# Kernel tuning notes

Hardware: AMD Instinct MI355X
Metric: run time of the kernel (lower is better)

Reference implementation:

```python
import jax, jax.numpy as jnp
import numpy as np

B, K, D, H, L = 128, 128, 768, 8, 4
HD = D // H
FF = 4 * D
SIM = D // 4
BOOST = 0.3
SCALE = HD ** -0.5
EPS = 1e-5


def _ln(x, g, b):
    m = x.mean(-1, keepdims=True)
    v = ((x - m) ** 2).mean(-1, keepdims=True)
    return (x - m) * jax.lax.rsqrt(v + EPS) * g + b


def setup_inputs() -> dict:
    key = jax.random.key(0)
    ks = jax.random.split(key, 10)
    def n(k, shape, s=0.02):
        return jax.random.normal(k, shape, dtype=jnp.float32) * s
    return {
        'slots': jax.random.normal(ks[0], (B, K, D), dtype=jnp.float32),
        'pos_emb': n(ks[1], (1, K, D)),
        'Wq': n(ks[2], (L, D, D)),
        'Wk': n(ks[3], (L, D, D)),
        'Wv': n(ks[4], (L, D, D)),
        'Wo': n(ks[5], (L, D, D)),
        'bo': jnp.zeros((L, D), jnp.float32),
        'Wsim': n(ks[6], (L, D, SIM)),
        'g1': jnp.ones((L, D), jnp.float32),
        'b1': jnp.zeros((L, D), jnp.float32),
        'g2': jnp.ones((L, D), jnp.float32),
        'b2': jnp.zeros((L, D), jnp.float32),
        'Wff1': n(ks[7], (L, D, FF)),
        'bff1': jnp.zeros((L, FF), jnp.float32),
        'Wff2': n(ks[8], (L, FF, D)),
        'bff2': jnp.zeros((L, D), jnp.float32),
        'gf': jnp.ones((D,), jnp.float32),
        'bf': jnp.zeros((D,), jnp.float32),
    }


def reference(slots, pos_emb, Wq, Wk, Wv, Wo, bo, Wsim, g1, b1, g2, b2,
              Wff1, bff1, Wff2, bff2, gf, bf):
    x = slots + pos_emb  # K == max_slots -> full pos table
    for l in range(L):
        # --- similarity-biased multi-head self-attention (pre-norm) ---
        nx = _ln(x, g1[l], b1[l])
        q = (nx @ Wq[l]).reshape(B, K, H, HD)
        k = (nx @ Wk[l]).reshape(B, K, H, HD)
        v = (nx @ Wv[l]).reshape(B, K, H, HD)
        scores = jnp.einsum('bqhd,bkhd->bhqk', q, k) * SCALE  # [B,H,K,K]
        s = nx @ Wsim[l]  # [B,K,D/4]
        s = s / jnp.maximum(jnp.linalg.norm(s, axis=-1, keepdims=True), 1e-12)
        sim = jnp.einsum('bqc,bkc->bqk', s, s)  # cosine similarity matrix
        scores = scores + BOOST * sim[:, None, :, :]
        a = jax.nn.softmax(scores, axis=-1)
        o = jnp.einsum('bhqk,bkhd->bqhd', a, v).reshape(B, K, D)
        x = x + (o @ Wo[l] + bo[l])
        # --- feed-forward (pre-norm) ---
        nx = _ln(x, g2[l], b2[l])
        h = jax.nn.gelu(nx @ Wff1[l] + bff1[l], approximate=False)
        x = x + (h @ Wff2[l] + bff2[l])
    return _ln(x, gf, bf)
```

## Files before the change

kernel.cpp:

```cpp
#include <hip/hip_runtime.h>

typedef unsigned short u16;
typedef unsigned int u32;
typedef float f32x4 __attribute__((ext_vector_type(4)));
typedef __bf16 bf16x8 __attribute__((ext_vector_type(8)));

static constexpr int D = 768, FFD = 3072, SIMC = 192, NH = 8, HD = 96;
static constexpr int B = 128, K = 128, M = B * K, NL = 4;
static constexpr int QKVW = 2560;
static constexpr int SIMOFF = 2304;
static constexpr float QSCALE = 0.14724502f;
static constexpr float SBOOST2 = 0.6578821f;
static constexpr float EPS_F = 1e-5f;

__device__ __forceinline__ float bf2f(u16 u) {
  union { u32 i; float f; } v; v.i = ((u32)u) << 16; return v.f;
}
__device__ __forceinline__ u16 f2bf(float f) {
  union { float f; u32 i; } v; v.f = f;
  u32 u = v.i;
  u32 r = (u + 0x7FFFu + ((u >> 16) & 1u)) >> 16;
  return (u16)r;
}

__device__ __forceinline__ float fast_gelu(float x) {
  float u2 = x * (2.3020585f + 0.102944f * x * x);
  float e = __builtin_amdgcn_exp2f(u2);
  float r = __builtin_amdgcn_rcpf(1.0f + e);
  return x - x * r;
}

__device__ __forceinline__ void gload16(const void* g, void* l) {
  __builtin_amdgcn_global_load_lds(
      (const __attribute__((address_space(1))) void*)g,
      (__attribute__((address_space(3))) void*)l, 16, 0, 0);
}

__global__ __launch_bounds__(256) void addpos_kernel(
    const float* __restrict__ slots, const float* __restrict__ pos,
    u16* __restrict__ x) {
  int i = blockIdx.x * 256 + threadIdx.x;
  int m = i / D;
  int d = i - m * D;
  x[i] = f2bf(slots[i] + pos[(m & (K - 1)) * D + d]);
}

__device__ __forceinline__ float block_sum(float v, float* sbuf) {
#pragma unroll
  for (int off = 32; off > 0; off >>= 1) v += __shfl_xor(v, off, 64);
  int lane = threadIdx.x & 63, w = threadIdx.x >> 6;
  if (lane == 0) sbuf[w] = v;
  __syncthreads();
  v = sbuf[0] + sbuf[1] + sbuf[2] + sbuf[3];
  __syncthreads();
  return v;
}

template <bool OUT_BF16>
__global__ __launch_bounds__(256) void ln_kernel(
    const u16* __restrict__ x, const float* __restrict__ g,
    const float* __restrict__ b, void* __restrict__ out) {
  __shared__ float sbuf[4];
  int row = blockIdx.x, tid = threadIdx.x;
  const u16* xr = x + (size_t)row * D;
  float v0 = bf2f(xr[tid]), v1 = bf2f(xr[tid + 256]), v2 = bf2f(xr[tid + 512]);
  float s = block_sum(v0 + v1 + v2, sbuf);
  float mean = s * (1.0f / D);
  float d0 = v0 - mean, d1 = v1 - mean, d2 = v2 - mean;
  float sq = block_sum(d0 * d0 + d1 * d1 + d2 * d2, sbuf);
  float rs = rsqrtf(sq * (1.0f / D) + EPS_F);
  float y0 = d0 * rs * g[tid] + b[tid];
  float y1 = d1 * rs * g[tid + 256] + b[tid + 256];
  float y2 = d2 * rs * g[tid + 512] + b[tid + 512];
  if (OUT_BF16) {
    u16* o = (u16*)out + (size_t)row * D;
    o[tid] = f2bf(y0); o[tid + 256] = f2bf(y1); o[tid + 512] = f2bf(y2);
  } else {
    float* o = (float*)out + (size_t)row * D;
    o[tid] = y0; o[tid + 256] = y1; o[tid + 512] = y2;
  }
}

struct WAll {
  const float *wq, *wk, *wv, *wo, *wsim, *wff1, *wff2;
  u16 *tA, *tB, *tC, *tD;
};
__global__ __launch_bounds__(256) void wconv_all_kernel(WAll p, float qscale) {
  __shared__ u16 t[32][33];
  int bid = blockIdx.x;
  int l = bid / 7056, b = bid - l * 7056;
  const float* W; u16* Wt; int N, Kd, n0, k0;
  float sc = 1.0f;
  if (b < 2304) {
    int z = b / 576, rem = b - z * 576;
    N = 768; Kd = 768;
    n0 = (rem % 24) * 32; k0 = (rem / 24) * 32;
    if (z == 0) { W = p.wq + (size_t)l * 589824; Wt = p.tA + (size_t)l * 1966080; sc = qscale; }
    else if (z == 1) { W = p.wk + (size_t)l * 589824; Wt = p.tA + (size_t)l * 1966080 + 589824; }
    else if (z == 2) { W = p.wv + (size_t)l * 589824; Wt = p.tA + (size_t)l * 1966080 + 1179648; }
    else { W = p.wo + (size_t)l * 589824; Wt = p.tB + (size_t)l * 589824; }
  } else if (b < 2448) {
    int rem = b - 2304;
    W = p.wsim + (size_t)l * 147456;
    Wt = p.tA + (size_t)l * 1966080 + (size_t)SIMOFF * 768;
    N = SIMC; Kd = 768;
    n0 = (rem % 6) * 32; k0 = (rem / 6) * 32;
  } else if (b < 4752) {
    int rem = b - 2448;
    W = p.wff1 + (size_t)l * 2359296; Wt = p.tC + (size_t)l * 2359296;
    N = FFD; Kd = 768;
    n0 = (rem % 96) * 32; k0 = (rem / 96) * 32;
  } else {
    int rem = b - 4752;
    W = p.wff2 + (size_t)l * 2359296; Wt = p.tD + (size_t)l * 2359296;
    N = 768; Kd = FFD;
    n0 = (rem % 24) * 32; k0 = (rem / 24) * 32;
  }
  int tid = threadIdx.x;
  int c = tid & 31, r4 = tid >> 5;
#pragma unroll
  for (int i = 0; i < 4; ++i) {
    int r = r4 + i * 8;
    t[r][c] = f2bf(W[(size_t)(k0 + r) * N + n0 + c] * sc);
  }
  __syncthreads();
#pragma unroll
  for (int i = 0; i < 4; ++i) {
    int r = r4 + i * 8;
    Wt[(size_t)(n0 + r) * Kd + k0 + c] = t[c][r];
  }
}

template <bool BIAS, bool GELU_, bool RESID>
__global__ __launch_bounds__(512, 2) void gemm256_kernel(
    const u16* __restrict__ A, const u16* __restrict__ Bt,
    const float* __restrict__ bias, const u16* __restrict__ resid,
    u16* __restrict__ Cout, int N, int Kdim, int NBX) {
  __shared__ u16 lds[65536];
  int tid = threadIdx.x;
  int w = tid >> 6, lane = tid & 63;
  int wm = w >> 2, wn = w & 3;
  int lr = lane & 15, lg = lane >> 4;

  int nwg = gridDim.x;
  int cpx = nwg >> 3;
  int swz = (blockIdx.x & 7) * cpx + (blockIdx.x >> 3);
  int bx = swz % NBX, by = swz / NBX;
  int n0 = bx << 8, m0 = by << 8;

  int scol = ((lane & 7) ^ (lane >> 3)) << 3;
  size_t aOff = (size_t)((w << 4) + (lane >> 3)) * Kdim + scol;
  u16* ldsU = lds;

  auto stageA = [&](int buf, int h, int t) {
    const u16* g = A + (size_t)(m0 + (h << 7)) * Kdim + ((size_t)t << 6) + aOff;
    u16* l = ldsU + buf * 32768 + h * 8192 + (w << 10);
    gload16(g, l);
    gload16(g + ((size_t)Kdim << 3), l + 512);
  };
  auto stageB = [&](int buf, int h, int t) {
    const u16* g = Bt + (size_t)(n0 + (h << 7)) * Kdim + ((size_t)t << 6) + aOff;
    u16* l = ldsU + buf * 32768 + 16384 + h * 8192 + (w << 10);
    gload16(g, l);
    gload16(g + ((size_t)Kdim << 3), l + 512);
  };

  const u16* lA0p = ldsU;
  const u16* lB0p = ldsU + 16384;
  const u16* lA1p = ldsU + 32768;
  const u16* lB1p = ldsU + 49152;
  int arow = (wm * 128 + lr) * 64;
  int brow = (wn * 64 + lr) * 64;
  int swz0 = (((lg * 16)) ^ ((lr & 7) << 4)) >> 1;
  int swz1 = ((64 + lg * 16) ^ ((lr & 7) << 4)) >> 1;

  f32x4 acc[8][4] = {};
  bf16x8 ar[2][4], br[2][4];

#define READ_A_KS(BASE, MSEG, KS)                                            \
  do {                                                                       \
    _Pragma("unroll") for (int mm = 0; mm < 4; ++mm) {                       \
      const u16* p_ = (BASE) + arow + ((MSEG) * 64 + mm * 16) * 64;          \
      ar[KS][mm] = *(const bf16x8*)(p_ + ((KS) ? swz1 : swz0));              \
    }                                                                        \
  } while (0)
#define READ_B_KS(BASE, NSEG, KS)                                            \
  do {                                                                       \
    _Pragma("unroll") for (int nn = 0; nn < 2; ++nn) {                       \
      const u16* p_ = (BASE) + brow + ((NSEG) * 32 + nn * 16) * 64;          \
      br[KS][(NSEG) * 2 + nn] = *(const bf16x8*)(p_ + ((KS) ? swz1 : swz0)); \
    }                                                                        \
  } while (0)
#define MFMA_Q(MSEG, NSEG)                                                   \
  do {                                                                       \
    __builtin_amdgcn_s_setprio(1);                                           \
    _Pragma("unroll") for (int ks = 0; ks < 2; ++ks)                         \
      _Pragma("unroll") for (int mm = 0; mm < 4; ++mm)                       \
        _Pragma("unroll") for (int nn = 0; nn < 2; ++nn)                     \
          acc[(MSEG) * 4 + mm][(NSEG) * 2 + nn] =                            \
              __builtin_amdgcn_mfma_f32_16x16x32_bf16(                       \
                  ar[ks][mm], br[ks][(NSEG) * 2 + nn],                       \
                  acc[(MSEG) * 4 + mm][(NSEG) * 2 + nn], 0, 0, 0);           \
    __builtin_amdgcn_s_setprio(0);                                           \
  } while (0)
#define PSYNC()                                                              \
  do {                                                                       \
    __builtin_amdgcn_sched_barrier(0);                                       \
    asm volatile("s_waitcnt lgkmcnt(0)" ::: "memory");                       \
    __builtin_amdgcn_s_barrier();                                            \
    __builtin_amdgcn_sched_barrier(0);                                       \
  } while (0)
#define PSYNC_V(N)                                                           \
  do {                                                                       \
    __builtin_amdgcn_sched_barrier(0);                                       \
    asm volatile("s_waitcnt vmcnt(" #N ") lgkmcnt(0)" ::: "memory");         \
    __builtin_amdgcn_s_barrier();                                            \
    __builtin_amdgcn_sched_barrier(0);                                       \
  } while (0)

  int NK = Kdim >> 6, NI = NK >> 1;
  stageA(0, 0, 0); stageA(0, 1, 0); stageB(0, 0, 0); stageB(0, 1, 0);
  stageB(1, 0, 1); stageB(1, 1, 1);
  asm volatile("s_waitcnt vmcnt(4)" ::: "memory");
  __builtin_amdgcn_s_barrier();
  __builtin_amdgcn_sched_barrier(0);

  for (int i = 0; i < NI; ++i) {
    int t1 = 2 * i + 1, t2 = 2 * i + 2, t3 = 2 * i + 3;
    bool last = (i == NI - 1);
    stageA(1, 0, t1); stageA(1, 1, t1);
    READ_A_KS(lA0p, 0, 0); READ_B_KS(lB0p, 0, 0); READ_B_KS(lB0p, 1, 0);
    READ_A_KS(lA0p, 0, 1); READ_B_KS(lB0p, 0, 1); READ_B_KS(lB0p, 1, 1);
    MFMA_Q(0, 0); MFMA_Q(0, 1);
    PSYNC();
    if (!last) { stageB(0, 0, t2); stageB(0, 1, t2); }
    READ_A_KS(lA0p, 1, 0); READ_A_KS(lA0p, 1, 1);
    MFMA_Q(1, 0); MFMA_Q(1, 1);
    if (last) PSYNC_V(0);
    else      PSYNC_V(4);
    if (!last) { stageA(0, 0, t2); stageA(0, 1, t2); }
    READ_A_KS(lA1p, 0, 0); READ_B_KS(lB1p, 0, 0); READ_B_KS(lB1p, 1, 0);
    READ_A_KS(lA1p, 0, 1); READ_B_KS(lB1p, 0, 1); READ_B_KS(lB1p, 1, 1);
    MFMA_Q(0, 0); MFMA_Q(0, 1);
    PSYNC();
    if (!last) { stageB(1, 0, t3); stageB(1, 1, t3); }
    READ_A_KS(lA1p, 1, 0); READ_A_KS(lA1p, 1, 1);
    MFMA_Q(1, 0); MFMA_Q(1, 1);
    if (last) PSYNC();
    else      PSYNC_V(4);
  }

#pragma unroll
  for (int m = 0; m < 8; ++m) {
#pragma unroll
    for (int n = 0; n < 4; ++n) {
      int col = n0 + wn * 64 + n * 16 + lr;
      float bv = BIAS ? bias[col] : 0.0f;
#pragma unroll
      for (int r = 0; r < 4; ++r) {
        int row = m0 + wm * 128 + m * 16 + lg * 4 + r;
        float v = acc[m][n][r];
        if (BIAS) v += bv;
        if (GELU_) v = fast_gelu(v);
        if (RESID) v += bf2f(resid[(size_t)row * N + col]);
        Cout[(size_t)row * N + col] = f2bf(v);
      }
    }
  }
#undef READ_A_KS
#undef READ_B_KS
#undef MFMA_Q
#undef PSYNC
#undef PSYNC_V
}

__global__ __launch_bounds__(256) void simpre_kernel(
    const u16* __restrict__ qkvb, u16* __restrict__ psim) {
  __shared__ u16 sln[128][200];
  int b = blockIdx.x, tid = threadIdx.x;
  {
    int row = tid >> 1, half = tid & 1;
    const u16* sr = qkvb + ((size_t)(b * K + row)) * QKVW + SIMOFF + half * 96;
    u16 v[96];
    float sq = 0.f;
#pragma unroll
    for (int j = 0; j < 12; ++j) {
      uint4 u4 = *(const uint4*)(sr + j * 8);
      u32 uu[4] = {u4.x, u4.y, u4.z, u4.w};
#pragma unroll
      for (int t = 0; t < 4; ++t) {
        v[j * 8 + 2 * t] = (u16)(uu[t] & 0xffffu);
        v[j * 8 + 2 * t + 1] = (u16)(uu[t] >> 16);
      }
    }
#pragma unroll
    for (int j = 0; j < 96; ++j) { float f = bf2f(v[j]); sq += f * f; }
    sq += __shfl_xor(sq, 1, 64);
    float inv = SBOOST2 / fmaxf(sqrtf(sq), 1e-12f);
#pragma unroll
    for (int j = 0; j < 96; ++j) sln[row][half * 96 + j] = f2bf(bf2f(v[j]) * inv);
  }
  __syncthreads();
  int w = tid >> 6, lane = tid & 63;
  int lr = lane & 15, lg = lane >> 4;
  int q0 = 32 * w;
  f32x4 accs[2][8] = {};
#pragma unroll
  for (int ks = 0; ks < 6; ++ks) {
    bf16x8 af[2];
#pragma unroll
    for (int m = 0; m < 2; ++m)
      af[m] = *(const bf16x8*)(&sln[q0 + 16 * m + lr][ks * 32 + lg * 8]);
#pragma unroll
    for (int n = 0; n < 8; ++n) {
      bf16x8 bf = *(const bf16x8*)(&sln[16 * n + lr][ks * 32 + lg * 8]);
#pragma unroll
      for (int m = 0; m < 2; ++m)
        accs[m][n] = __builtin_amdgcn_mfma_f32_16x16x32_bf16(af[m], bf, accs[m][n], 0, 0, 0);
    }
  }
  u16* pb = psim + (size_t)b * K * K;
#pragma unroll
  for (int m = 0; m < 2; ++m)
#pragma unroll
    for (int n = 0; n < 8; ++n)
#pragma unroll
      for (int r = 0; r < 4; ++r)
        pb[(size_t)(q0 + 16 * m + 4 * lg + r) * K + 16 * n + lr] = f2bf(accs[m][n][r]);
}

__global__ __launch_bounds__(256) void attn_kernel(
    const u16* __restrict__ qkv, const u16* __restrict__ psim,
    u16* __restrict__ ob) {
  __shared__ u16 Vt[96][136];
  __shared__ u16 Pl[4][32][136];
  int bh = blockIdx.x, b = bh >> 3, h = bh & 7;
  int tid = threadIdx.x, w = tid >> 6, lane = tid & 63;
  int lr = lane & 15, lg = lane >> 4;
  const u16* qb = qkv + (size_t)b * K * QKVW + h * HD;
  const u16* kb = qb + D;
  const u16* vb = qb + 2 * D;
  for (int idx = tid; idx < 128 * 12; idx += 256) {
    int r = idx / 12, db = idx - r * 12;
    uint4 v4 = *(const uint4*)(vb + (size_t)r * QKVW + db * 8);
    u32 vv[4] = {v4.x, v4.y, v4.z, v4.w};
#pragma unroll
    for (int j = 0; j < 4; ++j) {
      Vt[db * 8 + 2 * j][r] = (u16)(vv[j] & 0xffffu);
      Vt[db * 8 + 2 * j + 1][r] = (u16)(vv[j] >> 16);
    }
  }
  u16* siml = &Pl[0][0][0];
  {
    const u16* pb = psim + (size_t)b * K * K;
    for (int c = tid; c < 2048; c += 256) {
      int r = c >> 4, cc = c & 15;
      *(uint4*)(siml + r * 136 + cc * 8) = *(const uint4*)(pb + r * 128 + cc * 8);
    }
  }
  __syncthreads();
  int q0 = 32 * w;
  f32x4 accs[2][8];
#pragma unroll
  for (int m = 0; m < 2; ++m)
#pragma unroll
    for (int n = 0; n < 8; ++n)
#pragma unroll
      for (int r = 0; r < 4; ++r)
        accs[m][n][r] = bf2f(siml[(q0 + 16 * m + 4 * lg + r) * 136 + 16 * n + lr]);
#pragma unroll
  for (int ks = 0; ks < 3; ++ks) {
    bf16x8 af[2];
#pragma unroll
    for (int m = 0; m < 2; ++m)
      af[m] = *(const bf16x8*)(qb + (size_t)(q0 + 16 * m + lr) * QKVW + ks * 32 + lg * 8);
#pragma unroll
    for (int n = 0; n < 8; ++n) {
      bf16x8 bf = *(const bf16x8*)(kb + (size_t)(16 * n + lr) * QKVW + ks * 32 + lg * 8);
#pragma unroll
      for (int m = 0; m < 2; ++m)
        accs[m][n] = __builtin_amdgcn_mfma_f32_16x16x32_bf16(af[m], bf, accs[m][n], 0, 0, 0);
    }
  }
#pragma unroll
  for (int m = 0; m < 2; ++m) {
    float mx[4] = {-3e38f, -3e38f, -3e38f, -3e38f};
#pragma unroll
    for (int n = 0; n < 8; ++n)
#pragma unroll
      for (int r = 0; r < 4; ++r) mx[r] = fmaxf(mx[r], accs[m][n][r]);
#pragma unroll
    for (int r = 0; r < 4; ++r) {
      mx[r] = fmaxf(mx[r], __shfl_xor(mx[r], 1, 64));
      mx[r] = fmaxf(mx[r], __shfl_xor(mx[r], 2, 64));
      mx[r] = fmaxf(mx[r], __shfl_xor(mx[r], 4, 64));
      mx[r] = fmaxf(mx[r], __shfl_xor(mx[r], 8, 64));
    }
    float sm[4] = {0.f, 0.f, 0.f, 0.f};
#pragma unroll
    for (int n = 0; n < 8; ++n)
#pragma unroll
      for (int r = 0; r < 4; ++r) {
        float e = __builtin_amdgcn_exp2f(accs[m][n][r] - mx[r]);
        accs[m][n][r] = e;
        sm[r] += e;
      }
#pragma unroll
    for (int r = 0; r < 4; ++r) {
      sm[r] += __shfl_xor(sm[r], 1, 64);
      sm[r] += __shfl_xor(sm[r], 2, 64);
      sm[r] += __shfl_xor(sm[r], 4, 64);
      sm[r] += __shfl_xor(sm[r], 8, 64);
    }
    float inv[4];
#pragma unroll
    for (int r = 0; r < 4; ++r) inv[r] = 1.0f / sm[r];
#pragma unroll
    for (int n = 0; n < 8; ++n)
#pragma unroll
      for (int r = 0; r < 4; ++r)
        Pl[w][16 * m + 4 * lg + r][16 * n + lr] = f2bf(accs[m][n][r] * inv[r]);
  }
  __syncthreads();
  f32x4 acco[2][6] = {};
#pragma unroll
  for (int ks = 0; ks < 4; ++ks) {
    bf16x8 pa[2];
#pragma unroll
    for (int m = 0; m < 2; ++m)
      pa[m] = *(const bf16x8*)(&Pl[w][16 * m + lr][ks * 32 + lg * 8]);
#pragma unroll
    for (int n = 0; n < 6; ++n) {
      bf16x8 bv = *(const bf16x8*)(&Vt[16 * n + lr][ks * 32 + lg * 8]);
#pragma unroll
      for (int m = 0; m < 2; ++m)
        acco[m][n] = __builtin_amdgcn_mfma_f32_16x16x32_bf16(pa[m], bv, acco[m][n], 0, 0, 0);
    }
  }
  u16* obb = ob + (size_t)b * K * D + h * HD;
#pragma unroll
  for (int m = 0; m < 2; ++m)
#pragma unroll
    for (int n = 0; n < 6; ++n)
#pragma unroll
      for (int r = 0; r < 4; ++r)
        obb[(size_t)(q0 + 16 * m + 4 * lg + r) * D + 16 * n + lr] = f2bf(acco[m][n][r]);
}

extern "C" void kernel_launch(void* const* d_in, const int* in_sizes, int n_in,
                              void* d_out, int out_size, void* d_ws, size_t ws_size,
                              hipStream_t stream) {
  (void)in_sizes; (void)n_in; (void)out_size;
  const float* slots = (const float*)d_in[0];
  const float* pos   = (const float*)d_in[1];
  const float* Wq    = (const float*)d_in[2];
  const float* Wk    = (const float*)d_in[3];
  const float* Wv    = (const float*)d_in[4];
  const float* Wo    = (const float*)d_in[5];
  const float* bo    = (const float*)d_in[6];
  const float* Wsim  = (const float*)d_in[7];
  const float* g1    = (const float*)d_in[8];
  const float* b1    = (const float*)d_in[9];
  const float* g2    = (const float*)d_in[10];
  const float* b2    = (const float*)d_in[11];
  const float* Wff1  = (const float*)d_in[12];
  const float* bff1  = (const float*)d_in[13];
  const float* Wff2  = (const float*)d_in[14];
  const float* bff2  = (const float*)d_in[15];
  const float* gf    = (const float*)d_in[16];
  const float* bfin  = (const float*)d_in[17];

  char* p = (char*)d_ws;
  u16*   x    = (u16*)p;   p += (size_t)M * D * 2;
  u16*   nx   = (u16*)p;   p += (size_t)M * D * 2;
  u16*   qkvb = (u16*)p;   p += (size_t)M * QKVW * 2;
  u16*   ob   = (u16*)p;   p += (size_t)M * D * 2;
  u16*   psim = (u16*)p;   p += (size_t)B * K * K * 2;
  u16*   wtA4 = (u16*)p;   p += (size_t)4 * QKVW * D * 2;
  u16*   wtB4 = (u16*)p;   p += (size_t)4 * D * D * 2;
  u16*   wtC4 = (u16*)p;   p += (size_t)4 * FFD * D * 2;
  u16*   wtD4 = (u16*)p;   p += (size_t)4 * D * FFD * 2;
  if ((size_t)(p - (char*)d_ws) > ws_size) return;
  u16* hb = qkvb;

  addpos_kernel<<<M * D / 256, 256, 0, stream>>>(slots, pos, x);
  WAll wp = {Wq, Wk, Wv, Wo, Wsim, Wff1, Wff2, wtA4, wtB4, wtC4, wtD4};
  wconv_all_kernel<<<28224, 256, 0, stream>>>(wp, QSCALE);

  int nbx_qkv = QKVW / 256, nwg_qkv = nbx_qkv * (M / 256);
  int nbx_o   = D / 256,    nwg_o   = nbx_o * (M / 256);
  int nbx_f1  = FFD / 256,  nwg_f1  = nbx_f1 * (M / 256);

  for (int l = 0; l < NL; ++l) {
    ln_kernel<true><<<M, 256, 0, stream>>>(x, g1 + l * D, b1 + l * D, nx);
    gemm256_kernel<false, false, false><<<nwg_qkv, 512, 0, stream>>>(
        nx, wtA4 + (size_t)l * QKVW * D, nullptr, nullptr, qkvb, QKVW, D, nbx_qkv);
    simpre_kernel<<<B, 256, 0, stream>>>(qkvb, psim);
    attn_kernel<<<B * NH, 256, 0, stream>>>(qkvb, psim, ob);
    gemm256_kernel<true, false, true><<<nwg_o, 512, 0, stream>>>(
        ob, wtB4 + (size_t)l * D * D, bo + l * D, x, x, D, D, nbx_o);
    ln_kernel<true><<<M, 256, 0, stream>>>(x, g2 + l * D, b2 + l * D, nx);
    gemm256_kernel<true, true, false><<<nwg_f1, 512, 0, stream>>>(
        nx, wtC4 + (size_t)l * FFD * D, bff1 + l * FFD, nullptr, hb, FFD, D, nbx_f1);
    gemm256_kernel<true, false, true><<<nwg_o, 512, 0, stream>>>(
        hb, wtD4 + (size_t)l * D * FFD, bff2 + l * D, x, x, D, FFD, nbx_o);
  }
  ln_kernel<false><<<M, 256, 0, stream>>>(x, gf, bfin, d_out);
}
```

Measured before the change: 1.395 ms.

## Load GEMM B operand directly from global memory into registers, bypassing LDS

```diff
diff --git a/kernel.cpp b/kernel.cpp
--- a/kernel.cpp
+++ b/kernel.cpp
@@ -136,7 +136,7 @@
     const u16* __restrict__ A, const u16* __restrict__ Bt,
     const float* __restrict__ bias, const u16* __restrict__ resid,
     u16* __restrict__ Cout, int N, int Kdim, int NBX) {
-  __shared__ u16 lds[65536];
+  __shared__ u16 lds[32768];
   int tid = threadIdx.x;
   int w = tid >> 6, lane = tid & 63;
   int wm = w >> 2, wn = w & 3;
@@ -154,23 +154,19 @@
 
   auto stageA = [&](int buf, int h, int t) {
     const u16* g = A + (size_t)(m0 + (h << 7)) * Kdim + ((size_t)t << 6) + aOff;
-    u16* l = ldsU + buf * 32768 + h * 8192 + (w << 10);
+    u16* l = ldsU + buf * 16384 + h * 8192 + (w << 10);
     gload16(g, l);
     gload16(g + ((size_t)Kdim << 3), l + 512);
   };
-  auto stageB = [&](int buf, int h, int t) {
-    const u16* g = Bt + (size_t)(n0 + (h << 7)) * Kdim + ((size_t)t << 6) + aOff;
-    u16* l = ldsU + buf * 32768 + 16384 + h * 8192 + (w << 10);
-    gload16(g, l);
-    gload16(g + ((size_t)Kdim << 3), l + 512);
-  };
-
-  const u16* lA0p = ldsU;
-  const u16* lB0p = ldsU + 16384;
-  const u16* lA1p = ldsU + 32768;
-  const u16* lB1p = ldsU + 49152;
+
+  const u16* Brow[4];
+#pragma unroll
+  for (int j = 0; j < 4; ++j) {
+    int nseg = j >> 1, nn = j & 1;
+    Brow[j] = Bt + (size_t)(n0 + wn * 64 + nseg * 32 + nn * 16 + lr) * Kdim + lg * 8;
+  }
+
   int arow = (wm * 128 + lr) * 64;
-  int brow = (wn * 64 + lr) * 64;
   int swz0 = (((lg * 16)) ^ ((lr & 7) << 4)) >> 1;
   int swz1 = ((64 + lg * 16) ^ ((lr & 7) << 4)) >> 1;
 
@@ -182,13 +178,6 @@
     _Pragma("unroll") for (int mm = 0; mm < 4; ++mm) {                       \
       const u16* p_ = (BASE) + arow + ((MSEG) * 64 + mm * 16) * 64;          \
       ar[KS][mm] = *(const bf16x8*)(p_ + ((KS) ? swz1 : swz0));              \
-    }                                                                        \
-  } while (0)
-#define READ_B_KS(BASE, NSEG, KS)                                            \
-  do {                                                                       \
-    _Pragma("unroll") for (int nn = 0; nn < 2; ++nn) {                       \
-      const u16* p_ = (BASE) + brow + ((NSEG) * 32 + nn * 16) * 64;          \
-      br[KS][(NSEG) * 2 + nn] = *(const bf16x8*)(p_ + ((KS) ? swz1 : swz0)); \
     }                                                                        \
   } while (0)
 #define MFMA_Q(MSEG, NSEG)                                                   \
@@ -203,51 +192,35 @@
                   acc[(MSEG) * 4 + mm][(NSEG) * 2 + nn], 0, 0, 0);           \
     __builtin_amdgcn_s_setprio(0);                                           \
   } while (0)
-#define PSYNC()                                                              \
+#define PSYNC_END()                                                          \
   do {                                                                       \
     __builtin_amdgcn_sched_barrier(0);                                       \
-    asm volatile("s_waitcnt lgkmcnt(0)" ::: "memory");                       \
+    asm volatile("s_waitcnt vmcnt(0) lgkmcnt(0)" ::: "memory");              \
     __builtin_amdgcn_s_barrier();                                            \
     __builtin_amdgcn_sched_barrier(0);                                       \
   } while (0)
-#define PSYNC_V(N)                                                           \
-  do {                                                                       \
-    __builtin_amdgcn_sched_barrier(0);                                       \
-    asm volatile("s_waitcnt vmcnt(" #N ") lgkmcnt(0)" ::: "memory");         \
-    __builtin_amdgcn_s_barrier();                                            \
-    __builtin_amdgcn_sched_barrier(0);                                       \
-  } while (0)
-
-  int NK = Kdim >> 6, NI = NK >> 1;
-  stageA(0, 0, 0); stageA(0, 1, 0); stageB(0, 0, 0); stageB(0, 1, 0);
-  stageB(1, 0, 1); stageB(1, 1, 1);
-  asm volatile("s_waitcnt vmcnt(4)" ::: "memory");
+
+  int NK = Kdim >> 6;
+  stageA(0, 0, 0); stageA(0, 1, 0);
+  asm volatile("s_waitcnt vmcnt(0)" ::: "memory");
   __builtin_amdgcn_s_barrier();
   __builtin_amdgcn_sched_barrier(0);
 
-  for (int i = 0; i < NI; ++i) {
-    int t1 = 2 * i + 1, t2 = 2 * i + 2, t3 = 2 * i + 3;
-    bool last = (i == NI - 1);
-    stageA(1, 0, t1); stageA(1, 1, t1);
-    READ_A_KS(lA0p, 0, 0); READ_B_KS(lB0p, 0, 0); READ_B_KS(lB0p, 1, 0);
-    READ_A_KS(lA0p, 0, 1); READ_B_KS(lB0p, 0, 1); READ_B_KS(lB0p, 1, 1);
+  for (int t = 0; t < NK; ++t) {
+    int cur = t & 1;
+    const u16* lA = ldsU + cur * 16384;
+#pragma unroll
+    for (int ks = 0; ks < 2; ++ks)
+#pragma unroll
+      for (int j = 0; j < 4; ++j)
+        br[ks][j] = *(const bf16x8*)(Brow[j] + t * 64 + ks * 32);
+    __builtin_amdgcn_sched_barrier(0);
+    if (t + 1 < NK) { stageA(cur ^ 1, 0, t + 1); stageA(cur ^ 1, 1, t + 1); }
+    READ_A_KS(lA, 0, 0); READ_A_KS(lA, 0, 1);
     MFMA_Q(0, 0); MFMA_Q(0, 1);
-    PSYNC();
-    if (!last) { stageB(0, 0, t2); stageB(0, 1, t2); }
-    READ_A_KS(lA0p, 1, 0); READ_A_KS(lA0p, 1, 1);
+    READ_A_KS(lA, 1, 0); READ_A_KS(lA, 1, 1);
     MFMA_Q(1, 0); MFMA_Q(1, 1);
-    if (last) PSYNC_V(0);
-    else      PSYNC_V(4);
-    if (!last) { stageA(0, 0, t2); stageA(0, 1, t2); }
-    READ_A_KS(lA1p, 0, 0); READ_B_KS(lB1p, 0, 0); READ_B_KS(lB1p, 1, 0);
-    READ_A_KS(lA1p, 0, 1); READ_B_KS(lB1p, 0, 1); READ_B_KS(lB1p, 1, 1);
-    MFMA_Q(0, 0); MFMA_Q(0, 1);
-    PSYNC();
-    if (!last) { stageB(1, 0, t3); stageB(1, 1, t3); }
-    READ_A_KS(lA1p, 1, 0); READ_A_KS(lA1p, 1, 1);
-    MFMA_Q(1, 0); MFMA_Q(1, 1);
-    if (last) PSYNC();
-    else      PSYNC_V(4);
+    PSYNC_END();
   }
 
 #pragma unroll
@@ -268,10 +241,8 @@
     }
   }
 #undef READ_A_KS
-#undef READ_B_KS
 #undef MFMA_Q
-#undef PSYNC
-#undef PSYNC_V
+#undef PSYNC_END
 }
 
 __global__ __launch_bounds__(256) void simpre_kernel(
```

After: 2.149 ms. +54.0%, slower.
